# Kernel tuning notes

Measured on AMD Instinct MI355X. Metric: run time of the kernel, lower is better.

Reference implementation:

```python
import jax, jax.numpy as jnp
import numpy as np

N_RAYS = 16384
T = 4194304          # total ragged samples across all rays (avg 256/ray)
M_PAD = 512          # static pad width, >= max per-ray count
STEPSIZE = 3.0 * np.sqrt(3.0) / 1024.0  # (aabb extent)*sqrt(3)/render_n_samples


def setup_inputs() -> dict:
    key = jax.random.key(0)
    k1, k2, k3 = jax.random.split(key, 3)
    rays = jax.random.normal(k1, (N_RAYS, 6), dtype=jnp.float32)
    dirs = rays[:, 3:6]
    dirs = dirs / jnp.linalg.norm(dirs, axis=-1, keepdims=True)
    rays_chunk = jnp.concatenate([rays[:, 0:3], dirs], axis=-1)
    # ragged sample list from ray_marching: sorted ray ids -> ragged counts
    ray_indices = jnp.sort(jax.random.randint(k2, (T,), 0, N_RAYS, dtype=jnp.int32))
    t_starts = jax.random.uniform(k3, (T,), jnp.float32, 0.1, 5.0)
    t_ends = t_starts + jnp.float32(STEPSIZE)
    return {"rays_chunk": rays_chunk, "ray_indices": ray_indices,
            "t_starts": t_starts, "t_ends": t_ends, "max_samps": M_PAD}


def reference(rays_chunk, ray_indices, t_starts, t_ends, max_samps):
    N = rays_chunk.shape[0]
    Tn = ray_indices.shape[0]
    origins = rays_chunk[:, 0:3]
    viewdirs = rays_chunk[:, 3:6]

    pz_vals = (t_starts + t_ends) * 0.5              # [T]
    pdists = t_ends - t_starts                       # [T]
    xyz = origins[ray_indices] + pz_vals[:, None] * viewdirs[ray_indices]  # [T,3]
    # append 0 size channel -> (M, 4) premasked valid sample points
    xyz_sampled = jnp.concatenate([xyz, jnp.zeros((Tn, 1), xyz.dtype)], axis=-1)

    # per-ray counts (== torch.unique(..., return_counts=True) scattered to N)
    counts = jax.ops.segment_sum(jnp.ones((Tn,), jnp.int32), ray_indices,
                                 num_segments=N)                 # [N]
    offsets = jnp.cumsum(counts) - counts                        # exclusive cumsum
    pos = jnp.arange(Tn, dtype=jnp.int32) - offsets[ray_indices] # slot within ray

    ray_valid = jnp.arange(max_samps)[None, :] < counts[:, None] # [N, M] bool

    # boolean-mask scatters dists[ray_valid]=pdists etc., done as indexed scatter
    z_vals = jnp.zeros((N, max_samps), t_starts.dtype).at[ray_indices, pos].set(pz_vals)
    dists = jnp.zeros((N, max_samps), t_starts.dtype).at[ray_indices, pos].set(pdists)
    xyz_sampled_w = jnp.zeros((N, max_samps, 4), xyz.dtype).at[ray_indices, pos].set(xyz_sampled)

    whole_valid = jnp.ones((N,), dtype=bool)
    # original returns (xyzs, ray_valid, M, z_vals, dists, whole_valid);
    # M is the static pad width here; xyz_sampled_w appended to keep the
    # padded-scatter path (the kernel-headroom op) live.
    return (xyz_sampled, ray_valid, z_vals, dists, whole_valid, xyz_sampled_w)
```

## Files before the change

### kernel.cpp

```cpp
#include <hip/hip_runtime.h>

#define M_PAD 512

typedef float f32x4 __attribute__((ext_vector_type(4)));

__device__ __forceinline__ int lower_bound_seeded(const int* __restrict__ ri,
                                                  int T, int N, int target,
                                                  int lane) {
    int guess = (int)(((long long)target * T) / N);
    int W = 4096;
    int lo = max(0, guess - W), hi = min(T, guess + W);
    while (true) {
        bool okLo = (lo == 0) || (ri[lo - 1] < target);
        bool okHi = (hi == T) || (ri[hi] >= target);
        if (okLo && okHi) break;
        W <<= 3;
        lo = max(0, guess - W); hi = min(T, guess + W);
    }
    while (hi - lo > 64) {
        int len = hi - lo;
        int probe = lo + (len * (lane + 1)) / 65;
        int v = ri[probe];
        unsigned long long m = __ballot(v < target);
        int k = __popcll(m);
        int nlo = (k == 0)  ? lo : lo + (len * k) / 65;
        int nhi = (k == 64) ? hi : lo + (len * (k + 1)) / 65;
        lo = nlo; hi = nhi;
    }
    int p = lo + lane;
    int v = (p < hi) ? ri[p] : 2147483647;
    unsigned long long m = __ballot(v < target);
    return lo + __popcll(m);
}

__global__ __launch_bounds__(1024)
void mono_kernel(const float* __restrict__ rays,
                 const int* __restrict__ ri,
                 const float* __restrict__ ts,
                 const float* __restrict__ te,
                 float* __restrict__ xyz_out,
                 float* __restrict__ ray_valid,
                 float* __restrict__ z_vals,
                 float* __restrict__ dists,
                 float* __restrict__ xyz_w,
                 float* __restrict__ whole_valid,
                 int N, int T) {
    const int r0 = blockIdx.x * 2;
    const int tid = threadIdx.x;
    const int wave = tid >> 6, lane = tid & 63;

    __shared__ int sh[3];
    if (wave < 3) {
        int lb = lower_bound_seeded(ri, T, N, r0 + wave, lane);
        if (lane == 0) sh[wave] = lb;
    }
    __syncthreads();

    const int k = tid >> 9;
    const int j = tid & (M_PAD - 1);
    const int r = r0 + k;
    const int s = sh[k];
    const int cnt = sh[k + 1] - s;
    const int idx = (r << 9) + j;

    float z = 0.0f, dd = 0.0f, v = 0.0f;
    f32x4 pt = {0.f, 0.f, 0.f, 0.f};

    if (j < cnt) {
        int i = s + j;
        float a = ts[i], bb = te[i];
        z  = (a + bb) * 0.5f;
        dd = bb - a;
        v  = 1.0f;
        const float* rc = rays + (size_t)r * 6;
        pt.x = fmaf(z, rc[3], rc[0]);
        pt.y = fmaf(z, rc[4], rc[1]);
        pt.z = fmaf(z, rc[5], rc[2]);
        __builtin_nontemporal_store(pt, reinterpret_cast<f32x4*>(xyz_out) + i);
    }

    __builtin_nontemporal_store(z,  &z_vals[idx]);
    __builtin_nontemporal_store(dd, &dists[idx]);
    __builtin_nontemporal_store(v,  &ray_valid[idx]);
    __builtin_nontemporal_store(pt, reinterpret_cast<f32x4*>(xyz_w) + idx);

    if (j == 0) whole_valid[r] = 1.0f;
}

extern "C" void kernel_launch(void* const* d_in, const int* in_sizes, int n_in,
                              void* d_out, int out_size, void* d_ws, size_t ws_size,
                              hipStream_t stream) {
    const float* rays = (const float*)d_in[0];
    const int*   ri   = (const int*)d_in[1];
    const float* ts   = (const float*)d_in[2];
    const float* te   = (const float*)d_in[3];
    const int N = in_sizes[0] / 6;
    const int T = in_sizes[1];

    float* out         = (float*)d_out;
    float* xyz_out     = out;
    float* ray_valid   = xyz_out + (size_t)T * 4;
    float* z_vals      = ray_valid + (size_t)N * M_PAD;
    float* dists       = z_vals + (size_t)N * M_PAD;
    float* whole_valid = dists + (size_t)N * M_PAD;
    float* xyz_w       = whole_valid + N;

    mono_kernel<<<N / 2, 1024, 0, stream>>>(rays, ri, ts, te,
                                            xyz_out, ray_valid, z_vals,
                                            dists, xyz_w, whole_valid, N, T);
}
```

Before: 69.20 us.

## Split each ray across two 256-thread blocks and vectorize padded stores via LDS

Changes the launch from 1024-thread blocks covering two rays to 256-thread blocks covering half a ray each, so there are four times as many blocks. The scalar z/dist/valid stores are staged through shared memory and written as 16-byte vector stores by three waves. The change aims for finer scheduling granularity and wider store transactions. In exchange, the two binary searches per ray now run twice (once per half-block) and an extra barrier is added.

```diff
diff --git a/kernel.cpp b/kernel.cpp
--- a/kernel.cpp
+++ b/kernel.cpp
@@ -33,7 +33,7 @@
     return lo + __popcll(m);
 }
 
-__global__ __launch_bounds__(1024)
+__global__ __launch_bounds__(256)
 void mono_kernel(const float* __restrict__ rays,
                  const int* __restrict__ ri,
                  const float* __restrict__ ts,
@@ -45,23 +45,24 @@
                  float* __restrict__ xyz_w,
                  float* __restrict__ whole_valid,
                  int N, int T) {
-    const int r0 = blockIdx.x * 2;
+    const int b = blockIdx.x;
+    const int r = b >> 1;
+    const int h = b & 1;
     const int tid = threadIdx.x;
     const int wave = tid >> 6, lane = tid & 63;
 
-    __shared__ int sh[3];
-    if (wave < 3) {
-        int lb = lower_bound_seeded(ri, T, N, r0 + wave, lane);
+    __shared__ int sh[2];
+    __shared__ float lz[256], ld[256], lv[256];
+
+    if (wave < 2) {
+        int lb = lower_bound_seeded(ri, T, N, r + wave, lane);
         if (lane == 0) sh[wave] = lb;
     }
     __syncthreads();
+    const int s = sh[0];
+    const int cnt = sh[1] - s;
 
-    const int k = tid >> 9;
-    const int j = tid & (M_PAD - 1);
-    const int r = r0 + k;
-    const int s = sh[k];
-    const int cnt = sh[k + 1] - s;
-    const int idx = (r << 9) + j;
+    const int j = h * 256 + tid;
 
     float z = 0.0f, dd = 0.0f, v = 0.0f;
     f32x4 pt = {0.f, 0.f, 0.f, 0.f};
@@ -78,13 +79,24 @@
         pt.z = fmaf(z, rc[5], rc[2]);
         __builtin_nontemporal_store(pt, reinterpret_cast<f32x4*>(xyz_out) + i);
     }
+    __builtin_nontemporal_store(pt,
+        reinterpret_cast<f32x4*>(xyz_w) + ((size_t)r << 9) + j);
 
-    __builtin_nontemporal_store(z,  &z_vals[idx]);
-    __builtin_nontemporal_store(dd, &dists[idx]);
-    __builtin_nontemporal_store(v,  &ray_valid[idx]);
-    __builtin_nontemporal_store(pt, reinterpret_cast<f32x4*>(xyz_w) + idx);
+    lz[tid] = z; ld[tid] = dd; lv[tid] = v;
+    if (j == 0) whole_valid[r] = 1.0f;
+    __syncthreads();
 
-    if (j == 0) whole_valid[r] = 1.0f;
+    const size_t gslot = ((size_t)r << 9) + h * 256;
+    if (wave == 0) {
+        f32x4 x = *reinterpret_cast<f32x4*>(&lz[lane << 2]);
+        __builtin_nontemporal_store(x, reinterpret_cast<f32x4*>(z_vals + gslot) + lane);
+    } else if (wave == 1) {
+        f32x4 x = *reinterpret_cast<f32x4*>(&ld[lane << 2]);
+        __builtin_nontemporal_store(x, reinterpret_cast<f32x4*>(dists + gslot) + lane);
+    } else if (wave == 2) {
+        f32x4 x = *reinterpret_cast<f32x4*>(&lv[lane << 2]);
+        __builtin_nontemporal_store(x, reinterpret_cast<f32x4*>(ray_valid + gslot) + lane);
+    }
 }
 
 extern "C" void kernel_launch(void* const* d_in, const int* in_sizes, int n_in,
@@ -105,7 +117,7 @@
     float* whole_valid = dists + (size_t)N * M_PAD;
     float* xyz_w       = whole_valid + N;
 
-    mono_kernel<<<N / 2, 1024, 0, stream>>>(rays, ri, ts, te,
-                                            xyz_out, ray_valid, z_vals,
-                                            dists, xyz_w, whole_valid, N, T);
+    mono_kernel<<<N * 2, 256, 0, stream>>>(rays, ri, ts, te,
+                                           xyz_out, ray_valid, z_vals,
+                                           dists, xyz_w, whole_valid, N, T);
 }
```

Result: slower. 75.83 us (+9.6%).
